# Kernel tuning notes

Hardware: AMD Instinct MI355X
Metric: run time of the kernel (lower is better)

## Reference

```python
import jax, jax.numpy as jnp
import numpy as np

N_PIX = 196608  # 12 * 128**2 (HEALPix nside=128)
F = 32          # filters (Fin == Fout for residual)
DM = 2          # depth multiplier


def _cheb_sep_conv(x, idx, wnb, wd, wp, b):
    """Separable Chebyshev graph conv.
    x: [B,N,F] maps; idx: [N,nb] neighbor indices; wnb: [N,nb] Laplacian weights;
    wd: [K,F,DM] depthwise Chebyshev weights; wp: [F*DM,Fout] pointwise; b: [Fout].
    """
    def L(t):  # sparse Laplacian apply via fixed-degree neighbor gather
        return jnp.einsum('bnjf,nj->bnf', t[:, idx, :], wnb)
    K = wd.shape[0]
    Ts = [x, L(x)]
    for _ in range(K - 2):  # Chebyshev recursion T_k = 2 L T_{k-1} - T_{k-2}
        Ts.append(2.0 * L(Ts[-1]) - Ts[-2])
    T = jnp.stack(Ts, 0)                      # [K,B,N,F]
    y = jnp.einsum('kbnf,kfd->bnfd', T, wd)   # depthwise over Chebyshev orders
    Bb, Nn, Ff, Dd = y.shape
    y = y.reshape(Bb, Nn, Ff * Dd)
    return y @ wp + b                         # pointwise mix to Fout


def _layernorm(x, gamma, beta, eps=1e-6):
    mu = jnp.mean(x, axis=-1, keepdims=True)
    var = jnp.mean(jnp.square(x - mu), axis=-1, keepdims=True)
    return (x - mu) * jax.lax.rsqrt(var + eps) * gamma + beta


def setup_inputs() -> dict:
    key = jax.random.key(0)
    ks = jax.random.split(key, 10)
    inp = {
        'maps': jax.random.normal(ks[0], (1, N_PIX, F), jnp.float32),
        'idx1': jax.random.randint(ks[1], (N_PIX, 8), 0, N_PIX, jnp.int32),
        'w1_nb': jax.random.normal(ks[2], (N_PIX, 8), jnp.float32) * 0.1,
        'idx2': jax.random.randint(ks[3], (N_PIX, 20), 0, N_PIX, jnp.int32),
        'w2_nb': jax.random.normal(ks[4], (N_PIX, 20), jnp.float32) * 0.1,
        'wd1': jax.random.normal(ks[5], (6, F, DM), jnp.float32) * 0.1,
        'wp1': jax.random.normal(ks[6], (F * DM, F), jnp.float32) * 0.1,
        'b1': jnp.zeros((F,), jnp.float32),
        'gamma1': jnp.ones((F,), jnp.float32),
        'beta1': jnp.zeros((F,), jnp.float32),
        'wd2': jax.random.normal(ks[7], (10, F, DM), jnp.float32) * 0.1,
        'wp2': jax.random.normal(ks[8], (F * DM, F), jnp.float32) * 0.1,
        'b2': jnp.zeros((F,), jnp.float32),
        'gamma2': jnp.ones((F,), jnp.float32),
        'beta2': jnp.zeros((F,), jnp.float32),
    }
    return inp


def reference(maps, idx1, w1_nb, idx2, w2_nb, wd1, wp1, b1, gamma1, beta1,
              wd2, wp2, b2, gamma2, beta2):
    res = maps
    x = _cheb_sep_conv(maps, idx1, w1_nb, wd1, wp1, b1)   # K=6, nb=8
    x = jax.nn.relu(x)
    x = _layernorm(x, gamma1, beta1)
    x = _cheb_sep_conv(x, idx2, w2_nb, wd2, wp2, b2)      # K=10, nb=20
    x = jax.nn.relu(x)
    x = _layernorm(x, gamma2, beta2)
    return x + res
```

## Files before the change

### kernel.cpp

```cpp
#include <hip/hip_runtime.h>

constexpr int NPIX = 196608;
constexpr int FF   = 32;
constexpr size_t SLOT = (size_t)NPIX * FF;

typedef short bf16x8 __attribute__((ext_vector_type(8)));
typedef float f32x4  __attribute__((ext_vector_type(4)));
typedef int   i32x4  __attribute__((ext_vector_type(4)));
typedef uint  u32x4  __attribute__((ext_vector_type(4)));

__device__ __forceinline__ float blo(uint u) {
    union { float f; uint i; } v; v.i = u << 16; return v.f;
}
__device__ __forceinline__ float bhi(uint u) {
    union { float f; uint i; } v; v.i = u & 0xffff0000u; return v.f;
}
__device__ __forceinline__ ushort f2b(float f) {
    union { float f; uint i; } v; v.f = f;
    uint r = v.i + 0x7fffu + ((v.i >> 16) & 1u);
    return (ushort)(r >> 16);
}
__device__ __forceinline__ uint pack2(float lo, float hi) {
    return ((uint)f2b(hi) << 16) | (uint)f2b(lo);
}

__global__ __launch_bounds__(256) void f2b_kernel(const float* __restrict__ src,
                                                  ushort* __restrict__ dst) {
    int i = (blockIdx.x * 256 + threadIdx.x) * 4;
    f32x4 v = __builtin_nontemporal_load(reinterpret_cast<const f32x4*>(src + i));
    ushort4 o;
    o.x = f2b(v.x); o.y = f2b(v.y); o.z = f2b(v.z); o.w = f2b(v.w);
    *reinterpret_cast<ushort4*>(dst + i) = o;
}

template<int NB, bool INIT>
__global__ __launch_bounds__(256, 4) void cheb_step4(
    const ushort* __restrict__ Tprev,
    const ushort* __restrict__ Told,
    ushort*       __restrict__ Tout,
    const int*    __restrict__ idx,
    const float*  __restrict__ wnb)
{
    int t = blockIdx.x * 256 + threadIdx.x;
    int n = t >> 2;
    int h = t & 3;

    const i32x4* ip = reinterpret_cast<const i32x4*>(idx + (size_t)n * NB);
    const f32x4* wv = reinterpret_cast<const f32x4*>(wnb + (size_t)n * NB);
    i32x4 I[NB / 4];
    f32x4 W[NB / 4];
#pragma unroll
    for (int j = 0; j < NB / 4; ++j) {
        I[j] = __builtin_nontemporal_load(ip + j);
        W[j] = __builtin_nontemporal_load(wv + j);
    }

    const u32x4* Tp = reinterpret_cast<const u32x4*>(Tprev);
    float s0 = 0.f, s1 = 0.f, s2 = 0.f, s3 = 0.f;
    float s4 = 0.f, s5 = 0.f, s6 = 0.f, s7 = 0.f;

#pragma unroll
    for (int j = 0; j < NB / 4; ++j) {
        i32x4 i4 = I[j]; f32x4 w4 = W[j];
#pragma unroll
        for (int e = 0; e < 4; ++e) {
            int   ii = (e == 0) ? i4.x : (e == 1) ? i4.y : (e == 2) ? i4.z : i4.w;
            float ww = (e == 0) ? w4.x : (e == 1) ? w4.y : (e == 2) ? w4.z : w4.w;
            u32x4 u = Tp[(size_t)ii * 4 + h];
            s0 += ww * blo(u.x); s1 += ww * bhi(u.x);
            s2 += ww * blo(u.y); s3 += ww * bhi(u.y);
            s4 += ww * blo(u.z); s5 += ww * bhi(u.z);
            s6 += ww * blo(u.w); s7 += ww * bhi(u.w);
        }
    }

    size_t base = (size_t)n * 4 + h;
    u32x4 o;
    if (INIT) {
        o.x = pack2(s0, s1); o.y = pack2(s2, s3);
        o.z = pack2(s4, s5); o.w = pack2(s6, s7);
    } else {
        u32x4 told = __builtin_nontemporal_load(
            reinterpret_cast<const u32x4*>(Told) + base);
        o.x = pack2(2.f * s0 - blo(told.x), 2.f * s1 - bhi(told.x));
        o.y = pack2(2.f * s2 - blo(told.y), 2.f * s3 - bhi(told.y));
        o.z = pack2(2.f * s4 - blo(told.z), 2.f * s5 - bhi(told.z));
        o.w = pack2(2.f * s6 - blo(told.w), 2.f * s7 - bhi(told.w));
    }
    __builtin_nontemporal_store(o, reinterpret_cast<u32x4*>(Tout) + base);
}

template<int K, bool RESIDUAL, bool OUT_BF16>
__global__ __launch_bounds__(256, 4) void finish_gemm(
    const ushort* __restrict__ chain,
    const float*  __restrict__ wd,
    const float*  __restrict__ wp,
    const float*  __restrict__ bias,
    const float*  __restrict__ gamma,
    const float*  __restrict__ beta,
    const float*  __restrict__ resid,
    void*         __restrict__ outp)
{
    constexpr int KW = K * 32;
    constexpr int WSTRIDE = KW + 8;
    __shared__ float swp[64 * 33];
    __shared__ __align__(16) ushort sW[32][WSTRIDE];

    int tid = threadIdx.x;
    int wv = tid >> 6, l = tid & 63;
    int r = l & 15, hi = l >> 4;
    int nbase = blockIdx.x * 64 + wv * 16;

    bf16x8 aF[K];
#pragma unroll
    for (int k = 0; k < K; ++k)
        aF[k] = __builtin_nontemporal_load(reinterpret_cast<const bf16x8*>(
            chain + (size_t)k * SLOT + (size_t)(nbase + r) * FF + hi * 8));

    for (int i = tid; i < 64 * 32; i += 256) {
        int u = i >> 5, g = i & 31;
        swp[u * 33 + g] = wp[i];
    }
    __syncthreads();

    for (int i = tid; i < 32 * KW; i += 256) {
        int g = i / KW, kf = i - g * KW;
        int f = kf & 31;
        float2 wdv = *reinterpret_cast<const float2*>(wd + (size_t)kf * 2);
        float w2 = wdv.x * swp[(2 * f) * 33 + g] + wdv.y * swp[(2 * f + 1) * 33 + g];
        sW[g][kf] = f2b(w2);
    }
    __syncthreads();

    f32x4 acc0 = {0.f, 0.f, 0.f, 0.f};
    f32x4 acc1 = {0.f, 0.f, 0.f, 0.f};
#pragma unroll
    for (int k = 0; k < K; ++k) {
        bf16x8 b0 = *reinterpret_cast<const bf16x8*>(&sW[r][k * 32 + hi * 8]);
        bf16x8 b1 = *reinterpret_cast<const bf16x8*>(&sW[16 + r][k * 32 + hi * 8]);
        acc0 = __builtin_amdgcn_mfma_f32_16x16x32_bf16(aF[k], b0, acc0, 0, 0, 0);
        acc1 = __builtin_amdgcn_mfma_f32_16x16x32_bf16(aF[k], b1, acc1, 0, 0, 0);
    }

    float bias_lo = bias[r],  bias_hi = bias[16 + r];
    float gam_lo  = gamma[r], gam_hi  = gamma[16 + r];
    float bet_lo  = beta[r],  bet_hi  = beta[16 + r];

#pragma unroll
    for (int v = 0; v < 4; ++v) {
        acc0[v] = fmaxf(acc0[v] + bias_lo, 0.f);
        acc1[v] = fmaxf(acc1[v] + bias_hi, 0.f);
    }
#pragma unroll
    for (int v = 0; v < 4; ++v) {
        float s1 = acc0[v] + acc1[v];
        float s2 = acc0[v] * acc0[v] + acc1[v] * acc1[v];
#pragma unroll
        for (int m = 1; m < 16; m <<= 1) {
            s1 += __shfl_xor(s1, m);
            s2 += __shfl_xor(s2, m);
        }
        float mu  = s1 * (1.f / 32.f);
        float var = s2 * (1.f / 32.f) - mu * mu;
        float rs  = rsqrtf(var + 1e-6f);
        int n = nbase + hi * 4 + v;
        size_t o0 = (size_t)n * FF + r;
        size_t o1 = o0 + 16;
        float z0 = (acc0[v] - mu) * rs * gam_lo + bet_lo;
        float z1 = (acc1[v] - mu) * rs * gam_hi + bet_hi;
        if (RESIDUAL) { z0 += resid[o0]; z1 += resid[o1]; }
        if (OUT_BF16) {
            ((ushort*)outp)[o0] = f2b(z0);
            ((ushort*)outp)[o1] = f2b(z1);
        } else {
            ((float*)outp)[o0] = z0;
            ((float*)outp)[o1] = z1;
        }
    }
}

extern "C" void kernel_launch(void* const* d_in, const int* in_sizes, int n_in,
                              void* d_out, int out_size, void* d_ws, size_t ws_size,
                              hipStream_t stream) {
    const float* maps = (const float*)d_in[0];
    const int*   idx1 = (const int*)  d_in[1];
    const float* w1nb = (const float*)d_in[2];
    const int*   idx2 = (const int*)  d_in[3];
    const float* w2nb = (const float*)d_in[4];
    const float* wd1  = (const float*)d_in[5];
    const float* wp1  = (const float*)d_in[6];
    const float* b1   = (const float*)d_in[7];
    const float* g1   = (const float*)d_in[8];
    const float* be1  = (const float*)d_in[9];
    const float* wd2  = (const float*)d_in[10];
    const float* wp2  = (const float*)d_in[11];
    const float* b2   = (const float*)d_in[12];
    const float* g2   = (const float*)d_in[13];
    const float* be2  = (const float*)d_in[14];
    float* out = (float*)d_out;

    ushort* slots = (ushort*)d_ws;
    ushort* B = slots;
    ushort* A = slots + 4 * SLOT;

    const int stepBlocks = NPIX * 4 / 256;
    const int cvtBlocks  = NPIX * FF / (256 * 4);
    const int finBlocks  = NPIX / 64;

    f2b_kernel<<<cvtBlocks, 256, 0, stream>>>(maps, A);
    cheb_step4<8, true><<<stepBlocks, 256, 0, stream>>>(A, nullptr, A + SLOT, idx1, w1nb);
    cheb_step4<8, false><<<stepBlocks, 256, 0, stream>>>(A + SLOT,     A,              A + 2 * SLOT, idx1, w1nb);
    cheb_step4<8, false><<<stepBlocks, 256, 0, stream>>>(A + 2 * SLOT, A + SLOT,       A + 3 * SLOT, idx1, w1nb);
    cheb_step4<8, false><<<stepBlocks, 256, 0, stream>>>(A + 3 * SLOT, A + 2 * SLOT,   A + 4 * SLOT, idx1, w1nb);
    cheb_step4<8, false><<<stepBlocks, 256, 0, stream>>>(A + 4 * SLOT, A + 3 * SLOT,   A + 5 * SLOT, idx1, w1nb);
    finish_gemm<6, false, true><<<finBlocks, 256, 0, stream>>>(A, wd1, wp1, b1, g1, be1, nullptr, B);

    cheb_step4<20, true><<<stepBlocks, 256, 0, stream>>>(B, nullptr, B + SLOT, idx2, w2nb);
    for (int k = 2; k <= 9; ++k)
        cheb_step4<20, false><<<stepBlocks, 256, 0, stream>>>(
            B + (size_t)(k - 1) * SLOT, B + (size_t)(k - 2) * SLOT,
            B + (size_t)k * SLOT, idx2, w2nb);
    finish_gemm<10, true, false><<<finBlocks, 256, 0, stream>>>(B, wd2, wp2, b2, g2, be2, maps, out);
}
```

Baseline: 796.3 us.

## Sort neighbor edges by source and sweep gathers in bucketed frontier order

Result: faster. 776.9 us (-2.4%).

```diff
diff --git a/kernel.cpp b/kernel.cpp
--- a/kernel.cpp
+++ b/kernel.cpp
@@ -27,10 +27,89 @@
 __global__ __launch_bounds__(256) void f2b_kernel(const float* __restrict__ src,
                                                   ushort* __restrict__ dst) {
     int i = (blockIdx.x * 256 + threadIdx.x) * 4;
-    f32x4 v = __builtin_nontemporal_load(reinterpret_cast<const f32x4*>(src + i));
+    f32x4 v = *reinterpret_cast<const f32x4*>(src + i);
     ushort4 o;
     o.x = f2b(v.x); o.y = f2b(v.y); o.z = f2b(v.z); o.w = f2b(v.w);
     *reinterpret_cast<ushort4*>(dst + i) = o;
+}
+
+template<int NB>
+__global__ __launch_bounds__(256) void sort_edges(
+    const int*   __restrict__ idx,
+    const float* __restrict__ wnb,
+    ulong*       __restrict__ edges)
+{
+    int n = blockIdx.x * 256 + threadIdx.x;
+    ulong a[NB];
+#pragma unroll
+    for (int j = 0; j < NB; ++j) {
+        union { float f; uint u; } w; w.f = wnb[(size_t)n * NB + j];
+        a[j] = ((ulong)(uint)idx[(size_t)n * NB + j] << 32) | (ulong)w.u;
+    }
+#pragma unroll
+    for (int r = 0; r < NB; ++r) {
+#pragma unroll
+        for (int i = (r & 1); i + 1 < NB; i += 2) {
+            if (a[i] > a[i + 1]) { ulong t = a[i]; a[i] = a[i + 1]; a[i + 1] = t; }
+        }
+    }
+#pragma unroll
+    for (int j = 0; j < NB; ++j)
+        edges[(size_t)n * NB + j] = a[j];
+}
+
+template<int NB, int NBUCK, bool INIT>
+__global__ __launch_bounds__(256, 4) void cheb_stepB(
+    const ushort* __restrict__ Tprev,
+    const ushort* __restrict__ Told,
+    ushort*       __restrict__ Tout,
+    const ulong*  __restrict__ edges)
+{
+    int t = blockIdx.x * 256 + threadIdx.x;
+    int n = t >> 2;
+    int h = t & 3;
+
+    const u32x4* Tp = reinterpret_cast<const u32x4*>(Tprev);
+    size_t ebase = (size_t)n * NB;
+
+    float s0 = 0.f, s1 = 0.f, s2 = 0.f, s3 = 0.f;
+    float s4 = 0.f, s5 = 0.f, s6 = 0.f, s7 = 0.f;
+
+    constexpr int BW = NPIX / NBUCK;
+    constexpr ulong SENTINEL = 0x7FFFFFFF00000000ull;
+
+    int p = 0;
+    ulong e = edges[ebase];
+#pragma unroll 1
+    for (int b = 1; b <= NBUCK; ++b) {
+        int frontier = b * BW;
+        while ((int)(e >> 32) < frontier) {
+            int src = (int)(e >> 32);
+            union { float f; uint u; } wv; wv.u = (uint)e;
+            float ww = wv.f;
+            u32x4 u = Tp[(size_t)src * 4 + h];
+            s0 += ww * blo(u.x); s1 += ww * bhi(u.x);
+            s2 += ww * blo(u.y); s3 += ww * bhi(u.y);
+            s4 += ww * blo(u.z); s5 += ww * bhi(u.z);
+            s6 += ww * blo(u.w); s7 += ww * bhi(u.w);
+            ++p;
+            e = (p < NB) ? edges[ebase + p] : SENTINEL;
+        }
+    }
+
+    size_t base = (size_t)n * 4 + h;
+    u32x4 o;
+    if (INIT) {
+        o.x = pack2(s0, s1); o.y = pack2(s2, s3);
+        o.z = pack2(s4, s5); o.w = pack2(s6, s7);
+    } else {
+        u32x4 told = reinterpret_cast<const u32x4*>(Told)[base];
+        o.x = pack2(2.f * s0 - blo(told.x), 2.f * s1 - bhi(told.x));
+        o.y = pack2(2.f * s2 - blo(told.y), 2.f * s3 - bhi(told.y));
+        o.z = pack2(2.f * s4 - blo(told.z), 2.f * s5 - bhi(told.z));
+        o.w = pack2(2.f * s6 - blo(told.w), 2.f * s7 - bhi(told.w));
+    }
+    reinterpret_cast<u32x4*>(Tout)[base] = o;
 }
 
 template<int NB, bool INIT>
@@ -50,10 +129,7 @@
     i32x4 I[NB / 4];
     f32x4 W[NB / 4];
 #pragma unroll
-    for (int j = 0; j < NB / 4; ++j) {
-        I[j] = __builtin_nontemporal_load(ip + j);
-        W[j] = __builtin_nontemporal_load(wv + j);
-    }
+    for (int j = 0; j < NB / 4; ++j) { I[j] = ip[j]; W[j] = wv[j]; }
 
     const u32x4* Tp = reinterpret_cast<const u32x4*>(Tprev);
     float s0 = 0.f, s1 = 0.f, s2 = 0.f, s3 = 0.f;
@@ -80,14 +156,13 @@
         o.x = pack2(s0, s1); o.y = pack2(s2, s3);
         o.z = pack2(s4, s5); o.w = pack2(s6, s7);
     } else {
-        u32x4 told = __builtin_nontemporal_load(
-            reinterpret_cast<const u32x4*>(Told) + base);
+        u32x4 told = reinterpret_cast<const u32x4*>(Told)[base];
         o.x = pack2(2.f * s0 - blo(told.x), 2.f * s1 - bhi(told.x));
         o.y = pack2(2.f * s2 - blo(told.y), 2.f * s3 - bhi(told.y));
         o.z = pack2(2.f * s4 - blo(told.z), 2.f * s5 - bhi(told.z));
         o.w = pack2(2.f * s6 - blo(told.w), 2.f * s7 - bhi(told.w));
     }
-    __builtin_nontemporal_store(o, reinterpret_cast<u32x4*>(Tout) + base);
+    reinterpret_cast<u32x4*>(Tout)[base] = o;
 }
 
 template<int K, bool RESIDUAL, bool OUT_BF16>
@@ -114,8 +189,8 @@
     bf16x8 aF[K];
 #pragma unroll
     for (int k = 0; k < K; ++k)
-        aF[k] = __builtin_nontemporal_load(reinterpret_cast<const bf16x8*>(
-            chain + (size_t)k * SLOT + (size_t)(nbase + r) * FF + hi * 8));
+        aF[k] = *reinterpret_cast<const bf16x8*>(
+            chain + (size_t)k * SLOT + (size_t)(nbase + r) * FF + hi * 8);
 
     for (int i = tid; i < 64 * 32; i += 256) {
         int u = i >> 5, g = i & 31;
@@ -202,23 +277,50 @@
     ushort* slots = (ushort*)d_ws;
     ushort* B = slots;
     ushort* A = slots + 4 * SLOT;
+    ulong* edges2 = (ulong*)(slots + 10 * SLOT);
+    ulong* edges1 = edges2 + (size_t)NPIX * 20;
+
+    const size_t needSorted = 10 * SLOT * 2 + (size_t)NPIX * 20 * 8 + (size_t)NPIX * 8 * 8;
+    const bool useSorted = ws_size >= needSorted;
 
     const int stepBlocks = NPIX * 4 / 256;
     const int cvtBlocks  = NPIX * FF / (256 * 4);
     const int finBlocks  = NPIX / 64;
+    const int sortBlocks = NPIX / 256;
+
+    if (useSorted) {
+        sort_edges<8><<<sortBlocks, 256, 0, stream>>>(idx1, w1nb, edges1);
+        sort_edges<20><<<sortBlocks, 256, 0, stream>>>(idx2, w2nb, edges2);
+    }
 
     f2b_kernel<<<cvtBlocks, 256, 0, stream>>>(maps, A);
-    cheb_step4<8, true><<<stepBlocks, 256, 0, stream>>>(A, nullptr, A + SLOT, idx1, w1nb);
-    cheb_step4<8, false><<<stepBlocks, 256, 0, stream>>>(A + SLOT,     A,              A + 2 * SLOT, idx1, w1nb);
-    cheb_step4<8, false><<<stepBlocks, 256, 0, stream>>>(A + 2 * SLOT, A + SLOT,       A + 3 * SLOT, idx1, w1nb);
-    cheb_step4<8, false><<<stepBlocks, 256, 0, stream>>>(A + 3 * SLOT, A + 2 * SLOT,   A + 4 * SLOT, idx1, w1nb);
-    cheb_step4<8, false><<<stepBlocks, 256, 0, stream>>>(A + 4 * SLOT, A + 3 * SLOT,   A + 5 * SLOT, idx1, w1nb);
+    if (useSorted) {
+        cheb_stepB<8, 8, true><<<stepBlocks, 256, 0, stream>>>(A, nullptr, A + SLOT, edges1);
+        cheb_stepB<8, 8, false><<<stepBlocks, 256, 0, stream>>>(A + SLOT,     A,            A + 2 * SLOT, edges1);
+        cheb_stepB<8, 8, false><<<stepBlocks, 256, 0, stream>>>(A + 2 * SLOT, A + SLOT,     A + 3 * SLOT, edges1);
+        cheb_stepB<8, 8, false><<<stepBlocks, 256, 0, stream>>>(A + 3 * SLOT, A + 2 * SLOT, A + 4 * SLOT, edges1);
+        cheb_stepB<8, 8, false><<<stepBlocks, 256, 0, stream>>>(A + 4 * SLOT, A + 3 * SLOT, A + 5 * SLOT, edges1);
+    } else {
+        cheb_step4<8, true><<<stepBlocks, 256, 0, stream>>>(A, nullptr, A + SLOT, idx1, w1nb);
+        cheb_step4<8, false><<<stepBlocks, 256, 0, stream>>>(A + SLOT,     A,            A + 2 * SLOT, idx1, w1nb);
+        cheb_step4<8, false><<<stepBlocks, 256, 0, stream>>>(A + 2 * SLOT, A + SLOT,     A + 3 * SLOT, idx1, w1nb);
+        cheb_step4<8, false><<<stepBlocks, 256, 0, stream>>>(A + 3 * SLOT, A + 2 * SLOT, A + 4 * SLOT, idx1, w1nb);
+        cheb_step4<8, false><<<stepBlocks, 256, 0, stream>>>(A + 4 * SLOT, A + 3 * SLOT, A + 5 * SLOT, idx1, w1nb);
+    }
     finish_gemm<6, false, true><<<finBlocks, 256, 0, stream>>>(A, wd1, wp1, b1, g1, be1, nullptr, B);
 
-    cheb_step4<20, true><<<stepBlocks, 256, 0, stream>>>(B, nullptr, B + SLOT, idx2, w2nb);
-    for (int k = 2; k <= 9; ++k)
-        cheb_step4<20, false><<<stepBlocks, 256, 0, stream>>>(
-            B + (size_t)(k - 1) * SLOT, B + (size_t)(k - 2) * SLOT,
-            B + (size_t)k * SLOT, idx2, w2nb);
+    if (useSorted) {
+        cheb_stepB<20, 12, true><<<stepBlocks, 256, 0, stream>>>(B, nullptr, B + SLOT, edges2);
+        for (int k = 2; k <= 9; ++k)
+            cheb_stepB<20, 12, false><<<stepBlocks, 256, 0, stream>>>(
+                B + (size_t)(k - 1) * SLOT, B + (size_t)(k - 2) * SLOT,
+                B + (size_t)k * SLOT, edges2);
+    } else {
+        cheb_step4<20, true><<<stepBlocks, 256, 0, stream>>>(B, nullptr, B + SLOT, idx2, w2nb);
+        for (int k = 2; k <= 9; ++k)
+            cheb_step4<20, false><<<stepBlocks, 256, 0, stream>>>(
+                B + (size_t)(k - 1) * SLOT, B + (size_t)(k - 2) * SLOT,
+                B + (size_t)k * SLOT, idx2, w2nb);
+    }
     finish_gemm<10, true, false><<<finBlocks, 256, 0, stream>>>(B, wd2, wp2, b2, g2, be2, maps, out);
 }
```
